# Performance work log

Measured on AMD Instinct MI355X. Metric: run time of the kernel, lower is better.

Reference implementation:

```python
import jax, jax.numpy as jnp
import numpy as np

KS = 7       # t_kernel_size
PAD = 3      # t_padding
IN_DIM = 64
D_K = 64
D_V = 64


def setup_inputs() -> dict:
    key = jax.random.key(0)
    ks = jax.random.split(key, 9)
    B, C, T, N = 8, IN_DIM, 128, 207
    scale = 1.0 / np.sqrt(C)
    return {
        "q": jax.random.normal(ks[0], (B, C, T, N), jnp.float32),
        "k": jax.random.normal(ks[1], (B, C, T, N), jnp.float32),
        "v": jax.random.normal(ks[2], (B, C, T, N), jnp.float32),
        "Wq": jax.random.normal(ks[3], (D_K, C), jnp.float32) * scale,
        "bq": jax.random.normal(ks[4], (D_K,), jnp.float32) * 0.01,
        "Wk": jax.random.normal(ks[5], (D_K, C), jnp.float32) * scale,
        "bk": jax.random.normal(ks[6], (D_K,), jnp.float32) * 0.01,
        "Wv": jax.random.normal(ks[7], (D_V, C), jnp.float32) * scale,
        "bv": jax.random.normal(ks[8], (D_V,), jnp.float32) * 0.01,
    }


def reference(q, k, v, Wq, bq, Wk, bk, Wv, bv):
    # 1x1 convs == per-position channel projections
    Q = jnp.einsum('bctn,oc->botn', q, Wq) + bq[None, :, None, None]
    K = jnp.einsum('bctn,oc->botn', k, Wk) + bk[None, :, None, None]
    V = jnp.einsum('bctn,oc->botn', v, Wv) + bv[None, :, None, None]
    # conv_k/conv_v zero-pad the time axis by PAD (padding=(t_padding, 0))
    Kp = jnp.pad(K, ((0, 0), (0, 0), (PAD, PAD), (0, 0)))
    Vp = jnp.pad(V, ((0, 0), (0, 0), (PAD, PAD), (0, 0)))
    T_in = q.shape[2]
    T_out = T_in + 2 * PAD - KS + 1  # stride=1, dilation=1 -> == T_in
    # unfold: sliding windows along time; [B, d, T_out, N, KS]
    Kw = jnp.stack([Kp[:, :, i:i + T_out, :] for i in range(KS)], axis=-1)
    Vw = jnp.stack([Vp[:, :, i:i + T_out, :] for i in range(KS)], axis=-1)
    # side='both': center-crop Q to T_out (offset == 0 here)
    off = (T_in - T_out) // 2
    Qs = Q[:, :, off:T_in - off, :]
    # per-channel windowed attention: scores [B, d, T_out, N, KS]
    scores = Qs[..., None] * Kw
    attn = jax.nn.softmax(scores, axis=-1)
    out = jnp.sum(attn * Vw, axis=-1)  # [B, d_v, T_out, N]
    return out
```

## Files before the change

### kernel.cpp

```cpp
#include <hip/hip_runtime.h>

typedef _Float16 half8 __attribute__((ext_vector_type(8)));
typedef float floatx4 __attribute__((ext_vector_type(4)));
typedef float f32x4 __attribute__((ext_vector_type(4)));
typedef unsigned int uint4v __attribute__((ext_vector_type(4)));

#define B_DIM 8
#define C_DIM 64
#define T_DIM 128
#define N_DIM 207
#define O_DIM 64
#define CSTR  (T_DIM * N_DIM)

__global__ void pack_w(const float* __restrict__ Wq,
                       const float* __restrict__ Wk,
                       const float* __restrict__ Wv,
                       _Float16* __restrict__ ws)
{
    int i = threadIdx.x + blockIdx.x * blockDim.x;
    const int per = O_DIM * C_DIM;
    for (int m = i; m < 3 * per; m += blockDim.x * gridDim.x) {
        int arr = m / per, rem = m % per;
        const float* W = (arr == 0) ? Wq : (arr == 1) ? Wk : Wv;
        ws[m] = (_Float16)W[rem];
    }
}


#define GLDS(gp_, lp_)                                                       \
    __builtin_amdgcn_global_load_lds(                                        \
        (const __attribute__((address_space(1))) void*)(gp_),                \
        (__attribute__((address_space(3))) void*)(lp_), 4, 0, 0)

#define STAGE(tg_, P_)                                                       \
    {                                                                        \
        const int tcl_  = min(max((tg_), 0), T_DIM - 1);                     \
        const int toff_ = tcl_ * N_DIM;                                      \
        _Pragma("unroll")                                                    \
        for (int arr_ = 0; arr_ < 3; ++arr_) {                               \
            const float* ab_ = (arr_ == 0) ? qb2 : (arr_ == 1) ? kb2 : vb2;  \
            _Pragma("unroll")                                                \
            for (int i_ = 0; i_ < 4; ++i_) {                                 \
                GLDS(ab_ + toff_ + col_off[i_],                              \
                     &xls[P_][arr_][wv * 4 + i_][0][0]);                     \
            }                                                                \
        }                                                                    \
    }

#define MKFRAG(P_, arr_, kk_, dst_)                                          \
    {                                                                        \
        const float* ch_ = &xls[P_][arr_][qd * 2 + (kk_) * 8][nq][0];        \
        f32x4 A_ = *(const f32x4*)(ch_);                                     \
        f32x4 B_ = *(const f32x4*)(ch_ + 64);                                \
        uint4v t_;                                                           \
        t_[0] = __builtin_bit_cast(unsigned int, __builtin_amdgcn_cvt_pkrtz(A_[0], A_[1])); \
        t_[1] = __builtin_bit_cast(unsigned int, __builtin_amdgcn_cvt_pkrtz(A_[2], A_[3])); \
        t_[2] = __builtin_bit_cast(unsigned int, __builtin_amdgcn_cvt_pkrtz(B_[0], B_[1])); \
        t_[3] = __builtin_bit_cast(unsigned int, __builtin_amdgcn_cvt_pkrtz(B_[2], B_[3])); \
        dst_ = __builtin_bit_cast(half8, t_);                                \
    }

#define MFMA16(a_, b_, c_) __builtin_amdgcn_mfma_f32_16x16x32_f16(a_, b_, c_, 0, 0, 0)

#define VMWAIT(N_) asm volatile("s_waitcnt vmcnt(" #N_ ")" ::: "memory")

#define STEP(r_, N_)                                                         \
    {                                                                        \
        __builtin_amdgcn_sched_barrier(0);                                   \
        VMWAIT(N_);                                                          \
        __builtin_amdgcn_s_barrier();                                        \
        __builtin_amdgcn_sched_barrier(0);                                   \
        if ((r_) <= 19) STAGE(t0 - 1 + (r_), ((r_) + 2) % 3)                 \
        __builtin_amdgcn_sched_barrier(0);                                   \
        half8 fk0, fk1, fv0, fv1;                                            \
        MKFRAG((r_) % 3, 1, 0, fk0)  MKFRAG((r_) % 3, 1, 1, fk1)             \
        MKFRAG((r_) % 3, 2, 0, fv0)  MKFRAG((r_) % 3, 2, 1, fv1)             \
        floatx4 aq = {0.f, 0.f, 0.f, 0.f};                                   \
        floatx4 ak = {0.f, 0.f, 0.f, 0.f};                                   \
        floatx4 av = {0.f, 0.f, 0.f, 0.f};                                   \
        ak = MFMA16(af[1][0], fk0, ak);  ak = MFMA16(af[1][1], fk1, ak);     \
        av = MFMA16(af[2][0], fv0, av);  av = MFMA16(af[2][1], fv1, av);     \
        if ((r_) >= 3 && (r_) <= 18) {                                       \
            half8 fq0, fq1;                                                  \
            MKFRAG((r_) % 3, 0, 0, fq0)  MKFRAG((r_) % 3, 0, 1, fq1)         \
            aq = MFMA16(af[0][0], fq0, aq);  aq = MFMA16(af[0][1], fq1, aq); \
        }                                                                    \
        const int  tg_   = t0 - 3 + (r_);                                    \
        const bool rowv_ = (tg_ >= 0) && (tg_ < T_DIM);                      \
        _Pragma("unroll")                                                    \
        for (int j = 0; j < 4; ++j) {                                        \
            Kw[j][(r_) % 7]  = rowv_ ? (ak[j] + bk_r[j]) : 0.f;              \
            Vw[j][(r_) % 7]  = rowv_ ? (av[j] + bv_r[j]) : 0.f;              \
            Qd4[j][(r_) % 4] = aq[j] + bq_r[j];                              \
        }                                                                    \
        if ((r_) >= 6) {                                                     \
            const int to_ = t0 + (r_) - 6;                                   \
            const int n_g = n0 + nq;                                         \
            if (n_g < N_DIM) {                                               \
                _Pragma("unroll")                                            \
                for (int j = 0; j < 4; ++j) {                                \
                    const float qv = Qd4[j][((r_) + 1) % 4] * 1.44269504f;   \
                    float s[7];                                              \
                    _Pragma("unroll")                                        \
                    for (int i = 0; i < 7; ++i)                              \
                        s[i] = qv * Kw[j][((r_) + 1 + i) % 7];               \
                    float mx = s[0];                                         \
                    _Pragma("unroll")                                        \
                    for (int i = 1; i < 7; ++i) mx = fmaxf(mx, s[i]);        \
                    float den = 0.f, num = 0.f;                              \
                    _Pragma("unroll")                                        \
                    for (int i = 0; i < 7; ++i) {                            \
                        float e = exp2f(s[i] - mx);                          \
                        den += e;                                            \
                        num = fmaf(e, Vw[j][((r_) + 1 + i) % 7], num);       \
                    }                                                        \
                    out[((size_t)(b * O_DIM + o0 + qd * 4 + j) * T_DIM + to_) * N_DIM + n_g] \
                        = num * __builtin_amdgcn_rcpf(den);                  \
                }                                                            \
            }                                                                \
        }                                                                    \
    }

__global__ __launch_bounds__(256, 3)
void attn_mfma(const float* __restrict__ q,
               const float* __restrict__ k,
               const float* __restrict__ v,
               const float* __restrict__ bq,
               const float* __restrict__ bk,
               const float* __restrict__ bv,
               const _Float16* __restrict__ wpk,
               float* __restrict__ out)
{
    __shared__ __align__(16) float xls[3][3][16][16][4];

    const int tid  = threadIdx.x;
    const int lane = tid & 63;
    const int wv   = tid >> 6;
    const int nq   = lane & 15;
    const int qd   = lane >> 4;

    const int bid = (int)blockIdx.x + 13 * ((int)blockIdx.y + 8 * (int)blockIdx.z);
    const int swz = (bid & 7) * 104 + (bid >> 3);
    const int nb  = swz % 13;
    const int tc  = (swz / 13) & 7;
    const int b   = swz / 104;

    const int t0 = tc * 16;
    const int o0 = wv * 16;
    const int n0 = nb * 16;

    const int cl   = lane & 3;
    const int nrow = lane >> 2;
    const int n_cl = min(n0 + nrow, N_DIM - 1);
    int col_off[4];
    #pragma unroll
    for (int i = 0; i < 4; ++i)
        col_off[i] = ((wv * 4 + i) * 4 + cl) * CSTR + n_cl;

    const float* qb2 = q + (size_t)b * C_DIM * CSTR;
    const float* kb2 = k + (size_t)b * C_DIM * CSTR;
    const float* vb2 = v + (size_t)b * C_DIM * CSTR;

    half8 af[3][2];
    #pragma unroll
    for (int arr = 0; arr < 3; ++arr)
        #pragma unroll
        for (int kk = 0; kk < 2; ++kk)
            af[arr][kk] = *(const half8*)(wpk + ((size_t)(arr * 64 + o0 + nq) * 64
                                                 + qd * 8 + kk * 32));

    float bq_r[4], bk_r[4], bv_r[4];
    #pragma unroll
    for (int j = 0; j < 4; ++j) {
        const int og = o0 + qd * 4 + j;
        bq_r[j] = bq[og]; bk_r[j] = bk[og]; bv_r[j] = bv[og];
    }

    float Kw[4][7], Vw[4][7], Qd4[4][4];
    #pragma unroll
    for (int j = 0; j < 4; ++j) {
        #pragma unroll
        for (int i = 0; i < 7; ++i) { Kw[j][i] = 0.f; Vw[j][i] = 0.f; }
        #pragma unroll
        for (int i = 0; i < 4; ++i) Qd4[j][i] = 0.f;
    }

    STAGE(t0 - 3, 0)
    STAGE(t0 - 2, 1)

    STEP( 0, 12)  STEP( 1, 12)  STEP( 2, 12)  STEP( 3, 12)
    STEP( 4, 12)  STEP( 5, 12)  STEP( 6, 12)  STEP( 7, 16)
    STEP( 8, 20)  STEP( 9, 20)  STEP(10, 20)  STEP(11, 20)
    STEP(12, 20)  STEP(13, 20)  STEP(14, 20)  STEP(15, 20)
    STEP(16, 20)  STEP(17, 20)  STEP(18, 20)  STEP(19, 20)
    STEP(20, 20)  STEP(21,  8)
}

extern "C" void kernel_launch(void* const* d_in, const int* in_sizes, int n_in,
                              void* d_out, int out_size, void* d_ws, size_t ws_size,
                              hipStream_t stream)
{
    const float* q  = (const float*)d_in[0];
    const float* k  = (const float*)d_in[1];
    const float* v  = (const float*)d_in[2];
    const float* Wq = (const float*)d_in[3];
    const float* bq = (const float*)d_in[4];
    const float* Wk = (const float*)d_in[5];
    const float* bk = (const float*)d_in[6];
    const float* Wv = (const float*)d_in[7];
    const float* bv = (const float*)d_in[8];
    float* o = (float*)d_out;

    _Float16* ws_h = (_Float16*)d_ws;

    hipLaunchKernelGGL(pack_w, dim3(3), dim3(256), 0, stream, Wq, Wk, Wv, ws_h);

    dim3 grid(13, 8, B_DIM);
    dim3 block(256);
    hipLaunchKernelGGL(attn_mfma, grid, block, 0, stream,
                       q, k, v, bq, bk, bv, (const _Float16*)ws_h, o);
}
```

Measured before the change: 250.5 us.

## Process two time rows per barrier with double-buffered LDS superstages

Restructures the per-row pipeline (22 steps, each with its own barrier over a 3-slot ring buffer) into 11 supersteps that each stage and consume two time rows, using a 2x2 LDS buffer. This halves the number of workgroup barriers and vmcnt waits. In exchange the prefetch distance is shorter: the early supersteps wait with vmcnt(0), which can expose global load latency. LDS use grows from 3 to 4 row slots, which may affect occupancy.

```diff
diff --git a/kernel.cpp b/kernel.cpp
--- a/kernel.cpp
+++ b/kernel.cpp
@@ -32,7 +32,7 @@
         (const __attribute__((address_space(1))) void*)(gp_),                \
         (__attribute__((address_space(3))) void*)(lp_), 4, 0, 0)
 
-#define STAGE(tg_, P_)                                                       \
+#define STAGE(tg_, P_, R_)                                                   \
     {                                                                        \
         const int tcl_  = min(max((tg_), 0), T_DIM - 1);                     \
         const int toff_ = tcl_ * N_DIM;                                      \
@@ -42,14 +42,14 @@
             _Pragma("unroll")                                                \
             for (int i_ = 0; i_ < 4; ++i_) {                                 \
                 GLDS(ab_ + toff_ + col_off[i_],                              \
-                     &xls[P_][arr_][wv * 4 + i_][0][0]);                     \
+                     &xls[P_][R_][arr_][wv * 4 + i_][0][0]);                 \
             }                                                                \
         }                                                                    \
     }
 
-#define MKFRAG(P_, arr_, kk_, dst_)                                          \
-    {                                                                        \
-        const float* ch_ = &xls[P_][arr_][qd * 2 + (kk_) * 8][nq][0];        \
+#define MKFRAG(P_, R_, arr_, kk_, dst_)                                      \
+    {                                                                        \
+        const float* ch_ = &xls[P_][R_][arr_][qd * 2 + (kk_) * 8][nq][0];    \
         f32x4 A_ = *(const f32x4*)(ch_);                                     \
         f32x4 B_ = *(const f32x4*)(ch_ + 64);                                \
         uint4v t_;                                                           \
@@ -64,17 +64,11 @@
 
 #define VMWAIT(N_) asm volatile("s_waitcnt vmcnt(" #N_ ")" ::: "memory")
 
-#define STEP(r_, N_)                                                         \
-    {                                                                        \
-        __builtin_amdgcn_sched_barrier(0);                                   \
-        VMWAIT(N_);                                                          \
-        __builtin_amdgcn_s_barrier();                                        \
-        __builtin_amdgcn_sched_barrier(0);                                   \
-        if ((r_) <= 19) STAGE(t0 - 1 + (r_), ((r_) + 2) % 3)                 \
-        __builtin_amdgcn_sched_barrier(0);                                   \
+#define ROWBODY(r_, P_, R_)                                                  \
+    {                                                                        \
         half8 fk0, fk1, fv0, fv1;                                            \
-        MKFRAG((r_) % 3, 1, 0, fk0)  MKFRAG((r_) % 3, 1, 1, fk1)             \
-        MKFRAG((r_) % 3, 2, 0, fv0)  MKFRAG((r_) % 3, 2, 1, fv1)             \
+        MKFRAG(P_, R_, 1, 0, fk0)  MKFRAG(P_, R_, 1, 1, fk1)                 \
+        MKFRAG(P_, R_, 2, 0, fv0)  MKFRAG(P_, R_, 2, 1, fv1)                 \
         floatx4 aq = {0.f, 0.f, 0.f, 0.f};                                   \
         floatx4 ak = {0.f, 0.f, 0.f, 0.f};                                   \
         floatx4 av = {0.f, 0.f, 0.f, 0.f};                                   \
@@ -82,7 +76,7 @@
         av = MFMA16(af[2][0], fv0, av);  av = MFMA16(af[2][1], fv1, av);     \
         if ((r_) >= 3 && (r_) <= 18) {                                       \
             half8 fq0, fq1;                                                  \
-            MKFRAG((r_) % 3, 0, 0, fq0)  MKFRAG((r_) % 3, 0, 1, fq1)         \
+            MKFRAG(P_, R_, 0, 0, fq0)  MKFRAG(P_, R_, 0, 1, fq1)             \
             aq = MFMA16(af[0][0], fq0, aq);  aq = MFMA16(af[0][1], fq1, aq); \
         }                                                                    \
         const int  tg_   = t0 - 3 + (r_);                                    \
@@ -121,6 +115,21 @@
         }                                                                    \
     }
 
+#define SUPERSTEP(s_, N_)                                                    \
+    {                                                                        \
+        __builtin_amdgcn_sched_barrier(0);                                   \
+        VMWAIT(N_);                                                          \
+        __builtin_amdgcn_s_barrier();                                        \
+        __builtin_amdgcn_sched_barrier(0);                                   \
+        if ((s_) <= 9) {                                                     \
+            STAGE(t0 - 1 + 2 * (s_), ((s_) + 1) & 1, 0)                      \
+            STAGE(t0     + 2 * (s_), ((s_) + 1) & 1, 1)                      \
+        }                                                                    \
+        __builtin_amdgcn_sched_barrier(0);                                   \
+        ROWBODY(2 * (s_),     (s_) & 1, 0)                                   \
+        ROWBODY(2 * (s_) + 1, (s_) & 1, 1)                                   \
+    }
+
 __global__ __launch_bounds__(256, 3)
 void attn_mfma(const float* __restrict__ q,
                const float* __restrict__ k,
@@ -131,7 +140,7 @@
                const _Float16* __restrict__ wpk,
                float* __restrict__ out)
 {
-    __shared__ __align__(16) float xls[3][3][16][16][4];
+    __shared__ __align__(16) float xls[2][2][3][16][16][4];
 
     const int tid  = threadIdx.x;
     const int lane = tid & 63;
@@ -185,15 +194,12 @@
         for (int i = 0; i < 4; ++i) Qd4[j][i] = 0.f;
     }
 
-    STAGE(t0 - 3, 0)
-    STAGE(t0 - 2, 1)
-
-    STEP( 0, 12)  STEP( 1, 12)  STEP( 2, 12)  STEP( 3, 12)
-    STEP( 4, 12)  STEP( 5, 12)  STEP( 6, 12)  STEP( 7, 16)
-    STEP( 8, 20)  STEP( 9, 20)  STEP(10, 20)  STEP(11, 20)
-    STEP(12, 20)  STEP(13, 20)  STEP(14, 20)  STEP(15, 20)
-    STEP(16, 20)  STEP(17, 20)  STEP(18, 20)  STEP(19, 20)
-    STEP(20, 20)  STEP(21,  8)
+    STAGE(t0 - 3, 0, 0)
+    STAGE(t0 - 2, 0, 1)
+
+    SUPERSTEP( 0, 0)  SUPERSTEP( 1, 0)  SUPERSTEP( 2, 0)  SUPERSTEP( 3, 0)
+    SUPERSTEP( 4, 8)  SUPERSTEP( 5, 8)  SUPERSTEP( 6, 8)  SUPERSTEP( 7, 8)
+    SUPERSTEP( 8, 8)  SUPERSTEP( 9, 8)  SUPERSTEP(10, 8)
 }
 
 extern "C" void kernel_launch(void* const* d_in, const int* in_sizes, int n_in,
```

New measurement: 253.9 us. About the same (+1.4%).

## Use 16-byte global-to-LDS loads with permuted channel layout for fragments

Applied to the files above, without the earlier changes.

Replaces the per-element 4-byte global_load_lds staging with 16-byte-per-lane loads, so each wave stages four consecutive n values per lane in one instruction instead of four. The LDS layout and the channel-to-slot mapping are permuted so that MFMA fragments can be built from scalar LDS reads at fixed strides. The last, partial n-block keeps a 4-byte clamped path, and the vmcnt wait counts are adjusted per path. This cuts the number of load instructions and waitcnt pressure, at the cost of more scalar LDS reads when building fragments and added branching on the tail block.

```diff
diff --git a/kernel.cpp b/kernel.cpp
--- a/kernel.cpp
+++ b/kernel.cpp
@@ -2,7 +2,6 @@
 
 typedef _Float16 half8 __attribute__((ext_vector_type(8)));
 typedef float floatx4 __attribute__((ext_vector_type(4)));
-typedef float f32x4 __attribute__((ext_vector_type(4)));
 typedef unsigned int uint4v __attribute__((ext_vector_type(4)));
 
 #define B_DIM 8
@@ -27,7 +26,12 @@
 }
 
 
-#define GLDS(gp_, lp_)                                                       \
+#define GLDS16(gp_, lp_)                                                     \
+    __builtin_amdgcn_global_load_lds(                                        \
+        (const __attribute__((address_space(1))) void*)(gp_),                \
+        (__attribute__((address_space(3))) void*)(lp_), 16, 0, 0)
+
+#define GLDS4(gp_, lp_)                                                      \
     __builtin_amdgcn_global_load_lds(                                        \
         (const __attribute__((address_space(1))) void*)(gp_),                \
         (__attribute__((address_space(3))) void*)(lp_), 4, 0, 0)
@@ -36,27 +40,34 @@
     {                                                                        \
         const int tcl_  = min(max((tg_), 0), T_DIM - 1);                     \
         const int toff_ = tcl_ * N_DIM;                                      \
-        _Pragma("unroll")                                                    \
-        for (int arr_ = 0; arr_ < 3; ++arr_) {                               \
-            const float* ab_ = (arr_ == 0) ? qb2 : (arr_ == 1) ? kb2 : vb2;  \
+        if (nb != 12) {                                                      \
             _Pragma("unroll")                                                \
-            for (int i_ = 0; i_ < 4; ++i_) {                                 \
-                GLDS(ab_ + toff_ + col_off[i_],                              \
-                     &xls[P_][arr_][wv * 4 + i_][0][0]);                     \
+            for (int arr_ = 0; arr_ < 3; ++arr_) {                           \
+                const float* ab_ = (arr_ == 0) ? qb2 : (arr_ == 1) ? kb2 : vb2; \
+                GLDS16(ab_ + toff_ + cof16, &xls[P_][arr_][wv * 256]);       \
             }                                                                \
-        }                                                                    \
-    }
-
-#define MKFRAG(P_, arr_, kk_, dst_)                                          \
+        } else {                                                             \
+            _Pragma("unroll")                                                \
+            for (int arr_ = 0; arr_ < 3; ++arr_) {                           \
+                const float* ab_ = (arr_ == 0) ? qb2 : (arr_ == 1) ? kb2 : vb2; \
+                _Pragma("unroll")                                            \
+                for (int s_ = 0; s_ < 4; ++s_)                               \
+                    GLDS4(ab_ + toff_ + cofd[s_],                            \
+                          &xls[P_][arr_][wv * 256 + s_ * 64]);               \
+            }                                                                \
+        }                                                                    \
+    }
+
+#define PKU(a_, b_) __builtin_bit_cast(unsigned int, __builtin_amdgcn_cvt_pkrtz((a_), (b_)))
+
+#define MKFRAG32(P_, arr_, kk_, dst_)                                        \
     {                                                                        \
-        const float* ch_ = &xls[P_][arr_][qd * 2 + (kk_) * 8][nq][0];        \
-        f32x4 A_ = *(const f32x4*)(ch_);                                     \
-        f32x4 B_ = *(const f32x4*)(ch_ + 64);                                \
+        const float* p_ = lrd + ((P_) * 3072 + (arr_) * 1024 + (kk_) * 512); \
         uint4v t_;                                                           \
-        t_[0] = __builtin_bit_cast(unsigned int, __builtin_amdgcn_cvt_pkrtz(A_[0], A_[1])); \
-        t_[1] = __builtin_bit_cast(unsigned int, __builtin_amdgcn_cvt_pkrtz(A_[2], A_[3])); \
-        t_[2] = __builtin_bit_cast(unsigned int, __builtin_amdgcn_cvt_pkrtz(B_[0], B_[1])); \
-        t_[3] = __builtin_bit_cast(unsigned int, __builtin_amdgcn_cvt_pkrtz(B_[2], B_[3])); \
+        t_[0] = PKU(p_[0],   p_[32]);                                        \
+        t_[1] = PKU(p_[64],  p_[96]);                                        \
+        t_[2] = PKU(p_[128], p_[160]);                                       \
+        t_[3] = PKU(p_[192], p_[224]);                                       \
         dst_ = __builtin_bit_cast(half8, t_);                                \
     }
 
@@ -64,17 +75,17 @@
 
 #define VMWAIT(N_) asm volatile("s_waitcnt vmcnt(" #N_ ")" ::: "memory")
 
-#define STEP(r_, N_)                                                         \
+#define STEP(r_, N16_, N4_)                                                  \
     {                                                                        \
         __builtin_amdgcn_sched_barrier(0);                                   \
-        VMWAIT(N_);                                                          \
+        if (nb != 12) { VMWAIT(N16_); } else { VMWAIT(N4_); }                \
         __builtin_amdgcn_s_barrier();                                        \
         __builtin_amdgcn_sched_barrier(0);                                   \
         if ((r_) <= 19) STAGE(t0 - 1 + (r_), ((r_) + 2) % 3)                 \
         __builtin_amdgcn_sched_barrier(0);                                   \
         half8 fk0, fk1, fv0, fv1;                                            \
-        MKFRAG((r_) % 3, 1, 0, fk0)  MKFRAG((r_) % 3, 1, 1, fk1)             \
-        MKFRAG((r_) % 3, 2, 0, fv0)  MKFRAG((r_) % 3, 2, 1, fv1)             \
+        MKFRAG32((r_) % 3, 1, 0, fk0)  MKFRAG32((r_) % 3, 1, 1, fk1)         \
+        MKFRAG32((r_) % 3, 2, 0, fv0)  MKFRAG32((r_) % 3, 2, 1, fv1)         \
         floatx4 aq = {0.f, 0.f, 0.f, 0.f};                                   \
         floatx4 ak = {0.f, 0.f, 0.f, 0.f};                                   \
         floatx4 av = {0.f, 0.f, 0.f, 0.f};                                   \
@@ -82,7 +93,7 @@
         av = MFMA16(af[2][0], fv0, av);  av = MFMA16(af[2][1], fv1, av);     \
         if ((r_) >= 3 && (r_) <= 18) {                                       \
             half8 fq0, fq1;                                                  \
-            MKFRAG((r_) % 3, 0, 0, fq0)  MKFRAG((r_) % 3, 0, 1, fq1)         \
+            MKFRAG32((r_) % 3, 0, 0, fq0)  MKFRAG32((r_) % 3, 0, 1, fq1)     \
             aq = MFMA16(af[0][0], fq0, aq);  aq = MFMA16(af[0][1], fq1, aq); \
         }                                                                    \
         const int  tg_   = t0 - 3 + (r_);                                    \
@@ -131,7 +142,7 @@
                const _Float16* __restrict__ wpk,
                float* __restrict__ out)
 {
-    __shared__ __align__(16) float xls[3][3][16][16][4];
+    __shared__ __align__(16) float xls[3][3][1024];
 
     const int tid  = threadIdx.x;
     const int lane = tid & 63;
@@ -149,13 +160,24 @@
     const int o0 = wv * 16;
     const int n0 = nb * 16;
 
-    const int cl   = lane & 3;
-    const int nrow = lane >> 2;
-    const int n_cl = min(n0 + nrow, N_DIM - 1);
-    int col_off[4];
-    #pragma unroll
-    for (int i = 0; i < 4; ++i)
-        col_off[i] = ((wv * 4 + i) * 4 + cl) * CSTR + n_cl;
+    const int ladd = (qd & 1) * 64 + (qd >> 1) * 1024 + (nq >> 2) * 16 + (nq & 3) * 4;
+    const float* lrd = (const float*)&xls[0][0][0] + (ladd >> 2);
+
+    const int cs16 = wv * 16 + (lane >> 2);
+    const int cg16 = ((cs16 >> 5) << 5)
+                   + (((cs16 & 1) + ((cs16 >> 4) & 1) * 2) << 3)
+                   + ((cs16 >> 1) & 7);
+    const int cof16 = cg16 * CSTR + n0 + (lane & 3) * 4;
+    int cofd[4];
+    #pragma unroll
+    for (int s = 0; s < 4; ++s) {
+        const int cs = wv * 16 + s * 4 + (lane >> 4);
+        const int cg = ((cs >> 5) << 5)
+                     + (((cs & 1) + ((cs >> 4) & 1) * 2) << 3)
+                     + ((cs >> 1) & 7);
+        const int nn = min(n0 + ((lane >> 2) & 3) * 4 + (lane & 3), N_DIM - 1);
+        cofd[s] = cg * CSTR + nn;
+    }
 
     const float* qb2 = q + (size_t)b * C_DIM * CSTR;
     const float* kb2 = k + (size_t)b * C_DIM * CSTR;
@@ -188,12 +210,12 @@
     STAGE(t0 - 3, 0)
     STAGE(t0 - 2, 1)
 
-    STEP( 0, 12)  STEP( 1, 12)  STEP( 2, 12)  STEP( 3, 12)
-    STEP( 4, 12)  STEP( 5, 12)  STEP( 6, 12)  STEP( 7, 16)
-    STEP( 8, 20)  STEP( 9, 20)  STEP(10, 20)  STEP(11, 20)
-    STEP(12, 20)  STEP(13, 20)  STEP(14, 20)  STEP(15, 20)
-    STEP(16, 20)  STEP(17, 20)  STEP(18, 20)  STEP(19, 20)
-    STEP(20, 20)  STEP(21,  8)
+    STEP( 0,  3, 12)  STEP( 1,  3, 12)  STEP( 2,  3, 12)  STEP( 3,  3, 12)
+    STEP( 4,  3, 12)  STEP( 5,  3, 12)  STEP( 6,  3, 12)  STEP( 7,  7, 16)
+    STEP( 8, 11, 20)  STEP( 9, 11, 20)  STEP(10, 11, 20)  STEP(11, 11, 20)
+    STEP(12, 11, 20)  STEP(13, 11, 20)  STEP(14, 11, 20)  STEP(15, 11, 20)
+    STEP(16, 11, 20)  STEP(17, 11, 20)  STEP(18, 11, 20)  STEP(19, 11, 20)
+    STEP(20, 11, 20)  STEP(21,  8,  8)
 }
 
 extern "C" void kernel_launch(void* const* d_in, const int* in_sizes, int n_in,
```

Result: no change. 254.6 us (+1.6%).

## Split fused kernel into projection GEMM and windowed attention kernels

Applied to the files above, without the earlier changes.

Replaces the single fused projection-plus-attention kernel with two kernels when the workspace is large enough. The first computes Q/K/V 1x1-conv projections with MFMA and writes them to an fp16 intermediate. The second reads that buffer and computes the 7-tap per-channel windowed softmax with a sliding register window. This drops the fused kernel's redundant per-tile recomputation and barrier-heavy pipeline, at the cost of an extra global round trip of about 80 MB of fp16 intermediate data. The old fused kernel stays as a fallback when the workspace is too small.

```diff
diff --git a/kernel.cpp b/kernel.cpp
--- a/kernel.cpp
+++ b/kernel.cpp
@@ -11,6 +11,7 @@
 #define N_DIM 207
 #define O_DIM 64
 #define CSTR  (T_DIM * N_DIM)
+#define LOG2E 1.44269504f
 
 __global__ void pack_w(const float* __restrict__ Wq,
                        const float* __restrict__ Wk,
@@ -26,13 +27,178 @@
     }
 }
 
-
-#define GLDS(gp_, lp_)                                                       \
+#define GLDS4(gp_, lp_)                                                      \
     __builtin_amdgcn_global_load_lds(                                        \
         (const __attribute__((address_space(1))) void*)(gp_),                \
         (__attribute__((address_space(3))) void*)(lp_), 4, 0, 0)
 
-#define STAGE(tg_, P_)                                                       \
+#define MFMA16(a_, b_, c_) __builtin_amdgcn_mfma_f32_16x16x32_f16(a_, b_, c_, 0, 0, 0)
+#define PKU(a_, b_) __builtin_bit_cast(unsigned int, __builtin_amdgcn_cvt_pkrtz((a_), (b_)))
+
+__global__ __launch_bounds__(256, 4)
+void proj_gemm(const float* __restrict__ q,
+               const float* __restrict__ k,
+               const float* __restrict__ v,
+               const float* __restrict__ bq,
+               const float* __restrict__ bk,
+               const float* __restrict__ bv,
+               const _Float16* __restrict__ wpk,
+               _Float16* __restrict__ proj)
+{
+    __shared__ __align__(16) float xt[64 * 129 + 4];
+
+    const int tid = threadIdx.x, lane = tid & 63, wv = tid >> 6;
+    const int nq = lane & 15, qd = lane >> 4;
+    const int tile = blockIdx.x;
+    const int ab   = blockIdx.y;
+    const int arr  = ab >> 3, b = ab & 7;
+
+    const float* X    = ((arr == 0) ? q : (arr == 1) ? k : v) + (size_t)b * C_DIM * CSTR;
+    const float* bias = (arr == 0) ? bq : (arr == 1) ? bk : bv;
+    const int tn0 = tile * 128;
+
+    {
+        const float* s0 = X + tn0 + lane;
+        #pragma unroll
+        for (int i = 0; i < 16; ++i) {
+            const int c = wv * 16 + i;
+            GLDS4(s0 + (size_t)c * CSTR,      &xt[c * 129]);
+            GLDS4(s0 + (size_t)c * CSTR + 64, &xt[c * 129 + 64]);
+        }
+    }
+    __syncthreads();
+
+    const _Float16* wrow = wpk + ((size_t)(arr * 64 + wv * 16 + nq)) * 64 + qd * 8;
+    half8 af0 = *(const half8*)(wrow);
+    half8 af1 = *(const half8*)(wrow + 32);
+    float br[4];
+    #pragma unroll
+    for (int j = 0; j < 4; ++j) br[j] = bias[wv * 16 + qd * 4 + j];
+
+    floatx4 acc[8];
+    #pragma unroll
+    for (int f = 0; f < 8; ++f) acc[f] = (floatx4){0.f, 0.f, 0.f, 0.f};
+
+    const float* lb = &xt[qd * 8 * 129 + nq];
+    #pragma unroll
+    for (int f = 0; f < 8; ++f) {
+        #pragma unroll
+        for (int kk = 0; kk < 2; ++kk) {
+            const float* p = lb + kk * (32 * 129) + f * 16;
+            uint4v t_;
+            t_[0] = PKU(p[0 * 129], p[1 * 129]);
+            t_[1] = PKU(p[2 * 129], p[3 * 129]);
+            t_[2] = PKU(p[4 * 129], p[5 * 129]);
+            t_[3] = PKU(p[6 * 129], p[7 * 129]);
+            half8 fb = __builtin_bit_cast(half8, t_);
+            acc[f] = MFMA16((kk == 0) ? af0 : af1, fb, acc[f]);
+        }
+    }
+
+    #pragma unroll
+    for (int j = 0; j < 4; ++j) {
+        _Float16* rp = proj + ((size_t)(ab * 64 + wv * 16 + qd * 4 + j)) * CSTR
+                            + tn0 + nq;
+        #pragma unroll
+        for (int f = 0; f < 8; ++f)
+            rp[f * 16] = (_Float16)(acc[f][j] + br[j]);
+    }
+}
+
+__global__ __launch_bounds__(256, 4)
+void attn_win(const _Float16* __restrict__ proj, float* __restrict__ out)
+{
+    const int tid = threadIdx.x, lane = tid & 63, wv = tid >> 6;
+    const int og = blockIdx.x >> 3;
+    const int tc = blockIdx.x & 7;
+    const int nc = blockIdx.y;
+    const int b  = blockIdx.z;
+    const int o  = og * 4 + wv;
+    const int ta = tc * 16;
+    const int nn = nc * 128 + lane * 2;
+    const bool v0 = nn < N_DIM, v1 = nn + 1 < N_DIM;
+    const int off0 = min(nn,     N_DIM - 1);
+    const int off1 = min(nn + 1, N_DIM - 1);
+
+    const _Float16* Qp = proj + ((size_t)(b * 64 + o)) * CSTR;
+    const _Float16* Kp = Qp + (size_t)8  * 64 * CSTR;
+    const _Float16* Vp = Qp + (size_t)16 * 64 * CSTR;
+    float* Op = out + ((size_t)(b * 64 + o)) * CSTR + nn;
+
+#define LD2(base_, trow_, va_, a_, c_)                                       \
+    {                                                                        \
+        const _Float16* rp_ = (base_) + (size_t)(trow_) * N_DIM;             \
+        float x0_ = (float)rp_[off0];                                        \
+        float x1_ = (float)rp_[off1];                                        \
+        a_ = (va_) ? x0_ : 0.f;                                              \
+        c_ = (va_) ? x1_ : 0.f;                                              \
+    }
+
+    float k0[7], k1[7], w0[7], w1[7];
+    #pragma unroll
+    for (int i = 0; i < 6; ++i) {
+        const int tp  = ta - 3 + i;
+        const int tcl = min(max(tp, 0), T_DIM - 1);
+        const bool va = (tp >= 0) && (tp < T_DIM);
+        LD2(Kp, tcl, va, k0[i], k1[i]);
+        LD2(Vp, tcl, va, w0[i], w1[i]);
+    }
+
+    for (int i = 0; i < 16; ++i) {
+        const int t = ta + i;
+        {
+            const int tp  = t + 3;
+            const int tcl = min(tp, T_DIM - 1);
+            const bool va = tp < T_DIM;
+            LD2(Kp, tcl, va, k0[6], k1[6]);
+            LD2(Vp, tcl, va, w0[6], w1[6]);
+        }
+        float q0, q1;
+        LD2(Qp, t, true, q0, q1);
+        q0 *= LOG2E; q1 *= LOG2E;
+
+        float num0 = 0.f, den0 = 0.f, num1 = 0.f, den1 = 0.f;
+        {
+            float s[7];
+            #pragma unroll
+            for (int u = 0; u < 7; ++u) s[u] = q0 * k0[u];
+            float mx = s[0];
+            #pragma unroll
+            for (int u = 1; u < 7; ++u) mx = fmaxf(mx, s[u]);
+            #pragma unroll
+            for (int u = 0; u < 7; ++u) {
+                const float e = __builtin_amdgcn_exp2f(s[u] - mx);
+                den0 += e; num0 = fmaf(e, w0[u], num0);
+            }
+        }
+        {
+            float s[7];
+            #pragma unroll
+            for (int u = 0; u < 7; ++u) s[u] = q1 * k1[u];
+            float mx = s[0];
+            #pragma unroll
+            for (int u = 1; u < 7; ++u) mx = fmaxf(mx, s[u]);
+            #pragma unroll
+            for (int u = 0; u < 7; ++u) {
+                const float e = __builtin_amdgcn_exp2f(s[u] - mx);
+                den1 += e; num1 = fmaf(e, w1[u], num1);
+            }
+        }
+        if (v0) Op[(size_t)t * N_DIM]     = num0 * __builtin_amdgcn_rcpf(den0);
+        if (v1) Op[(size_t)t * N_DIM + 1] = num1 * __builtin_amdgcn_rcpf(den1);
+
+        #pragma unroll
+        for (int u = 0; u < 6; ++u) {
+            k0[u] = k0[u + 1]; k1[u] = k1[u + 1];
+            w0[u] = w0[u + 1]; w1[u] = w1[u + 1];
+        }
+    }
+#undef LD2
+}
+
+#define VMWAIT(N_) asm volatile("s_waitcnt vmcnt(" #N_ ")" ::: "memory")
+
+#define FSTAGE(tg_, P_)                                                      \
     {                                                                        \
         const int tcl_  = min(max((tg_), 0), T_DIM - 1);                     \
         const int toff_ = tcl_ * N_DIM;                                      \
@@ -41,40 +207,34 @@
             const float* ab_ = (arr_ == 0) ? qb2 : (arr_ == 1) ? kb2 : vb2;  \
             _Pragma("unroll")                                                \
             for (int i_ = 0; i_ < 4; ++i_) {                                 \
-                GLDS(ab_ + toff_ + col_off[i_],                              \
-                     &xls[P_][arr_][wv * 4 + i_][0][0]);                     \
+                GLDS4(ab_ + toff_ + col_off[i_],                             \
+                      &xls[P_][arr_][wv * 4 + i_][0][0]);                    \
             }                                                                \
         }                                                                    \
     }
 
-#define MKFRAG(P_, arr_, kk_, dst_)                                          \
+#define FMKFRAG(P_, arr_, kk_, dst_)                                         \
     {                                                                        \
         const float* ch_ = &xls[P_][arr_][qd * 2 + (kk_) * 8][nq][0];        \
         f32x4 A_ = *(const f32x4*)(ch_);                                     \
         f32x4 B_ = *(const f32x4*)(ch_ + 64);                                \
         uint4v t_;                                                           \
-        t_[0] = __builtin_bit_cast(unsigned int, __builtin_amdgcn_cvt_pkrtz(A_[0], A_[1])); \
-        t_[1] = __builtin_bit_cast(unsigned int, __builtin_amdgcn_cvt_pkrtz(A_[2], A_[3])); \
-        t_[2] = __builtin_bit_cast(unsigned int, __builtin_amdgcn_cvt_pkrtz(B_[0], B_[1])); \
-        t_[3] = __builtin_bit_cast(unsigned int, __builtin_amdgcn_cvt_pkrtz(B_[2], B_[3])); \
+        t_[0] = PKU(A_[0], A_[1]);  t_[1] = PKU(A_[2], A_[3]);               \
+        t_[2] = PKU(B_[0], B_[1]);  t_[3] = PKU(B_[2], B_[3]);               \
         dst_ = __builtin_bit_cast(half8, t_);                                \
     }
 
-#define MFMA16(a_, b_, c_) __builtin_amdgcn_mfma_f32_16x16x32_f16(a_, b_, c_, 0, 0, 0)
-
-#define VMWAIT(N_) asm volatile("s_waitcnt vmcnt(" #N_ ")" ::: "memory")
-
-#define STEP(r_, N_)                                                         \
+#define FSTEP(r_, N_)                                                        \
     {                                                                        \
         __builtin_amdgcn_sched_barrier(0);                                   \
         VMWAIT(N_);                                                          \
         __builtin_amdgcn_s_barrier();                                        \
         __builtin_amdgcn_sched_barrier(0);                                   \
-        if ((r_) <= 19) STAGE(t0 - 1 + (r_), ((r_) + 2) % 3)                 \
+        if ((r_) <= 19) FSTAGE(t0 - 1 + (r_), ((r_) + 2) % 3)                \
         __builtin_amdgcn_sched_barrier(0);                                   \
         half8 fk0, fk1, fv0, fv1;                                            \
-        MKFRAG((r_) % 3, 1, 0, fk0)  MKFRAG((r_) % 3, 1, 1, fk1)             \
-        MKFRAG((r_) % 3, 2, 0, fv0)  MKFRAG((r_) % 3, 2, 1, fv1)             \
+        FMKFRAG((r_) % 3, 1, 0, fk0)  FMKFRAG((r_) % 3, 1, 1, fk1)           \
+        FMKFRAG((r_) % 3, 2, 0, fv0)  FMKFRAG((r_) % 3, 2, 1, fv1)           \
         floatx4 aq = {0.f, 0.f, 0.f, 0.f};                                   \
         floatx4 ak = {0.f, 0.f, 0.f, 0.f};                                   \
         floatx4 av = {0.f, 0.f, 0.f, 0.f};                                   \
@@ -82,7 +242,7 @@
         av = MFMA16(af[2][0], fv0, av);  av = MFMA16(af[2][1], fv1, av);     \
         if ((r_) >= 3 && (r_) <= 18) {                                       \
             half8 fq0, fq1;                                                  \
-            MKFRAG((r_) % 3, 0, 0, fq0)  MKFRAG((r_) % 3, 0, 1, fq1)         \
+            FMKFRAG((r_) % 3, 0, 0, fq0)  FMKFRAG((r_) % 3, 0, 1, fq1)       \
             aq = MFMA16(af[0][0], fq0, aq);  aq = MFMA16(af[0][1], fq1, aq); \
         }                                                                    \
         const int  tg_   = t0 - 3 + (r_);                                    \
@@ -99,7 +259,7 @@
             if (n_g < N_DIM) {                                               \
                 _Pragma("unroll")                                            \
                 for (int j = 0; j < 4; ++j) {                                \
-                    const float qv = Qd4[j][((r_) + 1) % 4] * 1.44269504f;   \
+                    const float qv = Qd4[j][((r_) + 1) % 4] * LOG2E;         \
                     float s[7];                                              \
                     _Pragma("unroll")                                        \
                     for (int i = 0; i < 7; ++i)                              \
@@ -185,15 +345,15 @@
         for (int i = 0; i < 4; ++i) Qd4[j][i] = 0.f;
     }
 
-    STAGE(t0 - 3, 0)
-    STAGE(t0 - 2, 1)
-
-    STEP( 0, 12)  STEP( 1, 12)  STEP( 2, 12)  STEP( 3, 12)
-    STEP( 4, 12)  STEP( 5, 12)  STEP( 6, 12)  STEP( 7, 16)
-    STEP( 8, 20)  STEP( 9, 20)  STEP(10, 20)  STEP(11, 20)
-    STEP(12, 20)  STEP(13, 20)  STEP(14, 20)  STEP(15, 20)
-    STEP(16, 20)  STEP(17, 20)  STEP(18, 20)  STEP(19, 20)
-    STEP(20, 20)  STEP(21,  8)
+    FSTAGE(t0 - 3, 0)
+    FSTAGE(t0 - 2, 1)
+
+    FSTEP( 0, 12)  FSTEP( 1, 12)  FSTEP( 2, 12)  FSTEP( 3, 12)
+    FSTEP( 4, 12)  FSTEP( 5, 12)  FSTEP( 6, 12)  FSTEP( 7, 16)
+    FSTEP( 8, 20)  FSTEP( 9, 20)  FSTEP(10, 20)  FSTEP(11, 20)
+    FSTEP(12, 20)  FSTEP(13, 20)  FSTEP(14, 20)  FSTEP(15, 20)
+    FSTEP(16, 20)  FSTEP(17, 20)  FSTEP(18, 20)  FSTEP(19, 20)
+    FSTEP(20, 20)  FSTEP(21,  8)
 }
 
 extern "C" void kernel_launch(void* const* d_in, const int* in_sizes, int n_in,
@@ -212,11 +372,20 @@
     float* o = (float*)d_out;
 
     _Float16* ws_h = (_Float16*)d_ws;
-
     hipLaunchKernelGGL(pack_w, dim3(3), dim3(256), 0, stream, Wq, Wk, Wv, ws_h);
 
-    dim3 grid(13, 8, B_DIM);
-    dim3 block(256);
-    hipLaunchKernelGGL(attn_mfma, grid, block, 0, stream,
-                       q, k, v, bq, bk, bv, (const _Float16*)ws_h, o);
-}
+    const size_t PROJ_OFF = 32768;
+    const size_t NEED = PROJ_OFF + (size_t)3 * B_DIM * O_DIM * CSTR * sizeof(_Float16);
+
+    if (ws_size >= NEED) {
+        _Float16* proj = (_Float16*)((char*)d_ws + PROJ_OFF);
+        hipLaunchKernelGGL(proj_gemm, dim3(207, 24), dim3(256), 0, stream,
+                           q, k, v, bq, bk, bv, (const _Float16*)ws_h, proj);
+        hipLaunchKernelGGL(attn_win, dim3(128, 2, B_DIM), dim3(256), 0, stream,
+                           (const _Float16*)proj, o);
+    } else {
+        dim3 grid(13, 8, B_DIM);
+        hipLaunchKernelGGL(attn_mfma, grid, dim3(256), 0, stream,
+                           q, k, v, bq, bk, bv, (const _Float16*)ws_h, o);
+    }
+}
```

Result: slower. 259.8 us (+3.7%).
